# Optimization experiments

Hardware: AMD Instinct MI355X
Metric: run time of the kernel (lower is better)

## Reference

```python
import jax, jax.numpy as jnp
import numpy as np

N_NODES = 50000
N_EDGES = 600000
IN_DIM, HID, OUT_DIM = 128, 128, 64
LN_EPS = 1e-5


def setup_inputs() -> dict:
    key = jax.random.key(0)
    ks = jax.random.split(key, 10)
    def glorot(k, shape):
        lim = np.sqrt(6.0 / (shape[0] + shape[1]))
        return jax.random.uniform(k, shape, jnp.float32, -lim, lim)
    return {
        "x": jax.random.normal(ks[0], (N_NODES, IN_DIM), jnp.float32),
        "src": jax.random.randint(ks[1], (N_EDGES,), 0, N_NODES, jnp.int32),
        "dst": jax.random.randint(ks[2], (N_EDGES,), 0, N_NODES, jnp.int32),
        "W0": glorot(ks[3], (IN_DIM, HID)), "b0": jnp.zeros((HID,), jnp.float32),
        "W1": glorot(ks[4], (HID, HID)),    "b1": jnp.zeros((HID,), jnp.float32),
        "W2": glorot(ks[5], (HID, OUT_DIM)),"b2": jnp.zeros((OUT_DIM,), jnp.float32),
        "ln_scale": jnp.ones((HID,), jnp.float32),
        "ln_bias": jnp.zeros((HID,), jnp.float32),
    }


def _degree_norms(src, dst):
    ones = jnp.ones((src.shape[0],), jnp.float32)
    deg_out = jax.ops.segment_sum(ones, src, num_segments=N_NODES)
    deg_in = jax.ops.segment_sum(ones, dst, num_segments=N_NODES)
    # DGL clamps degree to min 1 for norm='both'
    out_norm = jnp.clip(deg_out, 1.0, None) ** -0.5
    in_norm = jnp.clip(deg_in, 1.0, None) ** -0.5
    return out_norm, in_norm


def _graph_conv(h, src, dst, out_norm, in_norm, W, b):
    # norm='both': scale src side, SpMM aggregate, scale dst side, then affine
    h = h * out_norm[:, None]
    h = h @ W  # apply weight first (mathematically identical, smaller messages when out<in)
    agg = jax.ops.segment_sum(h[src], dst, num_segments=N_NODES)  # [N, D]
    return agg * in_norm[:, None] + b


def _layernorm(h, scale, bias):
    mu = jnp.mean(h, axis=-1, keepdims=True)
    var = jnp.var(h, axis=-1, keepdims=True)
    return (h - mu) * jax.lax.rsqrt(var + LN_EPS) * scale + bias


def reference(x, src, dst, W0, b0, W1, b1, W2, b2, ln_scale, ln_bias):
    out_norm, in_norm = _degree_norms(src, dst)
    # dropout is identity in eval mode
    h = jax.nn.relu(_graph_conv(x, src, dst, out_norm, in_norm, W0, b0))
    h = _layernorm(h, ln_scale, ln_bias)
    h = jax.nn.relu(_graph_conv(h, src, dst, out_norm, in_norm, W1, b1))
    h = _layernorm(h, ln_scale, ln_bias)
    # last layer: encoding=True -> keep activation; no norm after last layer
    h = jax.nn.relu(_graph_conv(h, src, dst, out_norm, in_norm, W2, b2))
    return h
```

## Files before the change

kernel.cpp:

```cpp
#include <hip/hip_runtime.h>
#include <hip/hip_fp16.h>

#define NN 50000
#define NE 600000
#define LN_EPS 1e-5f
#define SCAN_B 49
#define RANGES 8
#define RSZ 6250
#define CHUNKS 30
#define CSZ 20000
#define HB (CHUNKS * RANGES)
#define GB ((NN + 63) / 64)

typedef __attribute__((ext_vector_type(8))) _Float16 half8;
typedef __attribute__((ext_vector_type(4))) float floatx4;

__device__ __align__(16) __half g_h0[NN * 128];
__device__ __align__(16) __half g_h1[NN * 128];
__device__ float g_out_norm[NN];
__device__ float g_in_norm[NN];
__device__ int g_rowptr[NN + 1];
__device__ int g_esrc[NE];
__device__ int g_blocksum[SCAN_B];
__device__ int g_perm[NN];
__device__ int g_dhist[SCAN_B * 256];
__device__ int g_pout[CHUNKS * NN];
__device__ int g_pin[CHUNKS * NN];
__device__ int g_base[CHUNKS * NN];
__device__ unsigned g_bar_count = 0;
__device__ unsigned g_bar_gen = 0;

__device__ __forceinline__ __half* hbuf(int i) { return i ? g_h1 : g_h0; }

__device__ __forceinline__ void gridbar(unsigned* expected) {
    __syncthreads();
    if (threadIdx.x == 0) {
        __threadfence();
        unsigned prev = __hip_atomic_fetch_add(&g_bar_count, 1u, __ATOMIC_ACQ_REL,
                                               __HIP_MEMORY_SCOPE_AGENT);
        if (prev == gridDim.x - 1) {
            __hip_atomic_store(&g_bar_count, 0u, __ATOMIC_RELAXED, __HIP_MEMORY_SCOPE_AGENT);
            __hip_atomic_fetch_add(&g_bar_gen, 1u, __ATOMIC_RELEASE, __HIP_MEMORY_SCOPE_AGENT);
        } else {
            while (__hip_atomic_load(&g_bar_gen, __ATOMIC_ACQUIRE, __HIP_MEMORY_SCOPE_AGENT) ==
                   *expected)
                __builtin_amdgcn_s_sleep(8);
        }
        __threadfence();
    }
    __syncthreads();
    (*expected)++;
}

__global__ __launch_bounds__(256) void k1_kernel(const int* __restrict__ src,
                                                 const int* __restrict__ dst,
                                                 const float* __restrict__ x,
                                                 const float* __restrict__ W0) {
    __shared__ __align__(16) int s_buf[2 * RSZ];
    const int tid = threadIdx.x;
    if (blockIdx.x < HB) {
        int* h_out = s_buf;
        int* h_in = s_buf + RSZ;
        int c = blockIdx.x / RANGES, r = blockIdx.x % RANGES;
        int lo = r * RSZ;
        for (int i = tid; i < RSZ; i += 256) { h_out[i] = 0; h_in[i] = 0; }
        __syncthreads();
        const int4* s4 = (const int4*)(src + c * CSZ);
        const int4* d4 = (const int4*)(dst + c * CSZ);
        for (int i = tid; i < CSZ / 4; i += 256) {
            int4 s = s4[i], d = d4[i];
            int v;
            v = s.x - lo; if ((unsigned)v < RSZ) atomicAdd(&h_out[v], 1);
            v = s.y - lo; if ((unsigned)v < RSZ) atomicAdd(&h_out[v], 1);
            v = s.z - lo; if ((unsigned)v < RSZ) atomicAdd(&h_out[v], 1);
            v = s.w - lo; if ((unsigned)v < RSZ) atomicAdd(&h_out[v], 1);
            v = d.x - lo; if ((unsigned)v < RSZ) atomicAdd(&h_in[v], 1);
            v = d.y - lo; if ((unsigned)v < RSZ) atomicAdd(&h_in[v], 1);
            v = d.z - lo; if ((unsigned)v < RSZ) atomicAdd(&h_in[v], 1);
            v = d.w - lo; if ((unsigned)v < RSZ) atomicAdd(&h_in[v], 1);
        }
        __syncthreads();
        for (int i = tid; i < RSZ; i += 256) {
            g_pout[c * NN + lo + i] = h_out[i];
            g_pin[c * NN + lo + i]  = h_in[i];
        }
    } else {
        _Float16* Wl = (_Float16*)s_buf;
        for (int e = tid; e < 128 * 128; e += 256) {
            int k = e >> 7, n = e & 127;
            Wl[(((k >> 3) * 128 + n) << 3) + (k & 7)] = (_Float16)W0[e];
        }
        __syncthreads();
        const int gb = blockIdx.x - HB;
        const int wv = tid >> 6, lane = tid & 63;
        const int quad = lane >> 4, mrow = lane & 15;
        const int rowbase = gb * 64 + wv * 16;
        const int arow0 = rowbase + mrow;
        const int arow = (arow0 < NN) ? arow0 : (NN - 1);
        floatx4 acc[8] = {};
#pragma unroll
        for (int kk = 0; kk < 4; ++kk) {
            const int k0 = kk * 32 + quad * 8;
            const float4* ap = (const float4*)(x + (size_t)arow * 128 + k0);
            float4 f0 = ap[0], f1 = ap[1];
            half8 afrag;
            afrag[0] = (_Float16)f0.x; afrag[1] = (_Float16)f0.y;
            afrag[2] = (_Float16)f0.z; afrag[3] = (_Float16)f0.w;
            afrag[4] = (_Float16)f1.x; afrag[5] = (_Float16)f1.y;
            afrag[6] = (_Float16)f1.z; afrag[7] = (_Float16)f1.w;
#pragma unroll
            for (int nt = 0; nt < 8; ++nt) {
                half8 bfrag = *(const half8*)&Wl[(((kk * 4 + quad) * 128 + nt * 16 + mrow) << 3)];
                acc[nt] = __builtin_amdgcn_mfma_f32_16x16x32_f16(afrag, bfrag, acc[nt], 0, 0, 0);
            }
        }
        __half* C = hbuf(0);
#pragma unroll
        for (int r = 0; r < 4; ++r) {
            int crow = rowbase + quad * 4 + r;
            if (crow < NN) {
#pragma unroll
                for (int nt = 0; nt < 8; ++nt)
                    C[(size_t)crow * 128 + nt * 16 + mrow] = __float2half_rn(acc[nt][r]);
            }
        }
    }
}

__global__ __launch_bounds__(1024) void mid_kernel() {
    __shared__ int wsum[16], woff[16];
    __shared__ int bscan[64];
    __shared__ int hist[256];
    __shared__ int cursor[256];
    __shared__ int cwsum[4], cwoff[4];
    unsigned expected = __hip_atomic_load(&g_bar_gen, __ATOMIC_RELAXED, __HIP_MEMORY_SCOPE_AGENT);
    const int b = blockIdx.x, t = threadIdx.x;
    const int lane = t & 63, wv = t >> 6;
    const int n = b * 1024 + t;
    if (t < 256) hist[t] = 0;
    int si = 0;
    if (n < NN) {
        int so = 0;
#pragma unroll
        for (int c = 0; c < CHUNKS; ++c) { so += g_pout[c * NN + n]; si += g_pin[c * NN + n]; }
        g_out_norm[n] = rsqrtf((float)max(so, 1));
        g_in_norm[n]  = rsqrtf((float)max(si, 1));
    }
    __syncthreads();
    int bin = min(si, 255);
    if (n < NN) atomicAdd(&hist[bin], 1);
    int inc = si;
#pragma unroll
    for (int off = 1; off < 64; off <<= 1) {
        int p = __shfl_up(inc, off, 64);
        if (lane >= off) inc += p;
    }
    if (lane == 63) wsum[wv] = inc;
    __syncthreads();
    if (t < 256) g_dhist[b * 256 + t] = hist[t];
    if (t < 16) {
        int x = wsum[t], y = x;
#pragma unroll
        for (int off = 1; off < 16; off <<= 1) {
            int p = __shfl_up(y, off, 16);
            if (t >= off) y += p;
        }
        woff[t] = y - x;
        if (t == 15) g_blocksum[b] = y;
    }
    gridbar(&expected);
    if (t < 64) {
        int own = (t < SCAN_B) ? g_blocksum[t] : 0;
        int v = own;
#pragma unroll
        for (int off = 1; off < 64; off <<= 1) {
            int p = __shfl_up(v, off, 64);
            if (t >= off) v += p;
        }
        bscan[t] = v - own;
        if (b == 0 && t == SCAN_B - 1) g_rowptr[NN] = v;
    }
    __syncthreads();
    int excl = (inc - si) + woff[wv] + bscan[b];
    if (n < NN) {
        g_rowptr[n] = excl;
        int run = excl;
#pragma unroll
        for (int c = 0; c < CHUNKS; ++c) {
            g_base[c * NN + n] = run;
            run += g_pin[c * NN + n];
        }
    }
    int cur = 0, tot = 0;
    if (t < 256) {
        for (int b2 = 0; b2 < SCAN_B; ++b2) {
            int h = g_dhist[b2 * 256 + t];
            cur += (b2 < b) ? h : 0;
            tot += h;
        }
    }
    int cinc = tot;
#pragma unroll
    for (int off = 1; off < 64; off <<= 1) {
        int p = __shfl_up(cinc, off, 64);
        if (lane >= off) cinc += p;
    }
    if (t < 256 && lane == 63) cwsum[wv] = cinc;
    __syncthreads();
    if (t < 4) {
        int x = cwsum[t], y = x;
#pragma unroll
        for (int off = 1; off < 4; off <<= 1) {
            int p = __shfl_up(y, off, 4);
            if (t >= off) y += p;
        }
        cwoff[t] = y - x;
    }
    __syncthreads();
    if (t < 256) cursor[t] = (cinc - tot) + cwoff[wv] + cur;
    __syncthreads();
    if (n < NN) {
        int pos = atomicAdd(&cursor[bin], 1);
        g_perm[pos] = n;
    }
}

__global__ __launch_bounds__(256) void place_lds_kernel(const int* __restrict__ src,
                                                        const int* __restrict__ dst) {
    __shared__ int cur[RSZ];
    int c = blockIdx.x / RANGES, r = blockIdx.x % RANGES;
    int lo = r * RSZ;
    for (int i = threadIdx.x; i < RSZ; i += 256) cur[i] = g_base[c * NN + lo + i];
    __syncthreads();
    const int4* s4 = (const int4*)(src + c * CSZ);
    const int4* d4 = (const int4*)(dst + c * CSZ);
    for (int i = threadIdx.x; i < CSZ / 4; i += 256) {
        int4 s = s4[i], d = d4[i];
        int v, p;
        v = d.x - lo; if ((unsigned)v < RSZ) { p = atomicAdd(&cur[v], 1); g_esrc[p] = s.x; }
        v = d.y - lo; if ((unsigned)v < RSZ) { p = atomicAdd(&cur[v], 1); g_esrc[p] = s.y; }
        v = d.z - lo; if ((unsigned)v < RSZ) { p = atomicAdd(&cur[v], 1); g_esrc[p] = s.z; }
        v = d.w - lo; if ((unsigned)v < RSZ) { p = atomicAdd(&cur[v], 1); g_esrc[p] = s.w; }
    }
}

template <int N>
__global__ __launch_bounds__(256) void gemm_mfma(int a_ib, int c_ib,
                                                 const float* __restrict__ Wg, int M) {
    constexpr int NT = N / 16;
    constexpr int LOGN = (N == 128) ? 7 : 6;
    __shared__ _Float16 Wl[128 * N];

    const int tid = threadIdx.x;
    for (int e = tid; e < 128 * N; e += 256) {
        int k = e >> LOGN, n = e & (N - 1);
        Wl[(((k >> 3) * N + n) << 3) + (k & 7)] = (_Float16)Wg[e];
    }
    __syncthreads();

    const int wv = tid >> 6, lane = tid & 63;
    const int quad = lane >> 4, mrow = lane & 15;
    const int rowbase = blockIdx.x * 64 + wv * 16;
    const int arow0 = rowbase + mrow;
    const int arow = (arow0 < M) ? arow0 : (M - 1);

    floatx4 acc[NT] = {};
    const __half* Ah = hbuf(a_ib);

#pragma unroll
    for (int kk = 0; kk < 4; ++kk) {
        const int k0 = kk * 32 + quad * 8;
        half8 afrag = *(const half8*)(Ah + (size_t)arow * 128 + k0);
#pragma unroll
        for (int nt = 0; nt < NT; ++nt) {
            half8 bfrag = *(const half8*)&Wl[(((kk * 4 + quad) * N + nt * 16 + mrow) << 3)];
            acc[nt] = __builtin_amdgcn_mfma_f32_16x16x32_f16(afrag, bfrag, acc[nt], 0, 0, 0);
        }
    }

    __half* C = hbuf(c_ib);
#pragma unroll
    for (int r = 0; r < 4; ++r) {
        int crow = rowbase + quad * 4 + r;
        if (crow < M) {
            float s = g_out_norm[crow];
#pragma unroll
            for (int nt = 0; nt < NT; ++nt) {
                float v = acc[nt][r] * s;
                C[(size_t)crow * N + nt * 16 + mrow] = __float2half_rn(v);
            }
        }
    }
}

__device__ __forceinline__ void acc_row(uint4 u, float wt,
                                        float& a0, float& a1, float& a2, float& a3,
                                        float& a4, float& a5, float& a6, float& a7) {
    float2 f0 = __half22float2(*(const __half2*)&u.x);
    float2 f1 = __half22float2(*(const __half2*)&u.y);
    float2 f2 = __half22float2(*(const __half2*)&u.z);
    float2 f3 = __half22float2(*(const __half2*)&u.w);
    a0 = fmaf(wt, f0.x, a0); a1 = fmaf(wt, f0.y, a1);
    a2 = fmaf(wt, f1.x, a2); a3 = fmaf(wt, f1.y, a3);
    a4 = fmaf(wt, f2.x, a4); a5 = fmaf(wt, f2.y, a5);
    a6 = fmaf(wt, f3.x, a6); a7 = fmaf(wt, f3.y, a7);
}

template <bool SC>
__global__ __launch_bounds__(256) void gather_ln_kernel(int s_ib, int d_ib,
                                                        const float* __restrict__ b,
                                                        const float* __restrict__ ln_s,
                                                        const float* __restrict__ ln_b) {
    int wave = threadIdx.x >> 6;
    int lane = threadIdx.x & 63;
    int sub = lane >> 4, sl = lane & 15;
    int idx = blockIdx.x * 16 + wave * 4 + sub;
    int node = g_perm[idx];
    const uint4* Hu = (const uint4*)hbuf(s_ib);
    int beg = g_rowptr[node], end = g_rowptr[node + 1];
    float a0 = 0.f, a1 = 0.f, a2 = 0.f, a3 = 0.f, a4 = 0.f, a5 = 0.f, a6 = 0.f, a7 = 0.f;
    int j = beg;
    for (; j + 7 < end; j += 8) {
        int ss[8]; uint4 uu[8]; float ww[8];
#pragma unroll
        for (int q = 0; q < 8; ++q) ss[q] = g_esrc[j + q];
#pragma unroll
        for (int q = 0; q < 8; ++q) uu[q] = Hu[ss[q] * 16 + sl];
#pragma unroll
        for (int q = 0; q < 8; ++q) ww[q] = SC ? g_out_norm[ss[q]] : 1.0f;
#pragma unroll
        for (int q = 0; q < 8; ++q) acc_row(uu[q], ww[q], a0, a1, a2, a3, a4, a5, a6, a7);
    }
    for (; j + 3 < end; j += 4) {
        int ss[4]; uint4 uu[4]; float ww[4];
#pragma unroll
        for (int q = 0; q < 4; ++q) ss[q] = g_esrc[j + q];
#pragma unroll
        for (int q = 0; q < 4; ++q) uu[q] = Hu[ss[q] * 16 + sl];
#pragma unroll
        for (int q = 0; q < 4; ++q) ww[q] = SC ? g_out_norm[ss[q]] : 1.0f;
#pragma unroll
        for (int q = 0; q < 4; ++q) acc_row(uu[q], ww[q], a0, a1, a2, a3, a4, a5, a6, a7);
    }
    for (; j < end; ++j) {
        int s0 = g_esrc[j];
        float w0 = SC ? g_out_norm[s0] : 1.0f;
        acc_row(Hu[s0 * 16 + sl], w0, a0, a1, a2, a3, a4, a5, a6, a7);
    }
    float nrm = g_in_norm[node];
    float4 bA = ((const float4*)b)[sl * 2], bB = ((const float4*)b)[sl * 2 + 1];
    float v0 = fmaxf(a0 * nrm + bA.x, 0.f), v1 = fmaxf(a1 * nrm + bA.y, 0.f);
    float v2 = fmaxf(a2 * nrm + bA.z, 0.f), v3 = fmaxf(a3 * nrm + bA.w, 0.f);
    float v4 = fmaxf(a4 * nrm + bB.x, 0.f), v5 = fmaxf(a5 * nrm + bB.y, 0.f);
    float v6 = fmaxf(a6 * nrm + bB.z, 0.f), v7 = fmaxf(a7 * nrm + bB.w, 0.f);
    float s = ((v0 + v1) + (v2 + v3)) + ((v4 + v5) + (v6 + v7));
    float sq = ((v0 * v0 + v1 * v1) + (v2 * v2 + v3 * v3)) +
               ((v4 * v4 + v5 * v5) + (v6 * v6 + v7 * v7));
#pragma unroll
    for (int off = 8; off > 0; off >>= 1) {
        s  += __shfl_xor(s, off, 64);
        sq += __shfl_xor(sq, off, 64);
    }
    float mean = s * (1.f / 128.f);
    float var = sq * (1.f / 128.f) - mean * mean;
    float inv = rsqrtf(var + LN_EPS);
    float4 lsA = ((const float4*)ln_s)[sl * 2], lsB = ((const float4*)ln_s)[sl * 2 + 1];
    float4 lbA = ((const float4*)ln_b)[sl * 2], lbB = ((const float4*)ln_b)[sl * 2 + 1];
    __half2 h0 = __floats2half2_rn((v0 - mean) * inv * lsA.x + lbA.x, (v1 - mean) * inv * lsA.y + lbA.y);
    __half2 h1 = __floats2half2_rn((v2 - mean) * inv * lsA.z + lbA.z, (v3 - mean) * inv * lsA.w + lbA.w);
    __half2 h2 = __floats2half2_rn((v4 - mean) * inv * lsB.x + lbB.x, (v5 - mean) * inv * lsB.y + lbB.y);
    __half2 h3 = __floats2half2_rn((v6 - mean) * inv * lsB.z + lbB.z, (v7 - mean) * inv * lsB.w + lbB.w);
    uint4 o = make_uint4(*(const unsigned int*)&h0, *(const unsigned int*)&h1,
                         *(const unsigned int*)&h2, *(const unsigned int*)&h3);
    ((uint4*)hbuf(d_ib))[node * 16 + sl] = o;
}

__global__ __launch_bounds__(256) void GCN_63831803953156_kernel(int s_ib,
                                                                 const float* __restrict__ b2,
                                                                 float* __restrict__ out) {
    int wave = threadIdx.x >> 6;
    int lane = threadIdx.x & 63;
    int sub = lane >> 3, sl = lane & 7;
    int idx = blockIdx.x * 32 + wave * 8 + sub;
    if (idx >= NN) return;
    int node = g_perm[idx];
    const uint4* Hu = (const uint4*)hbuf(s_ib);
    int beg = g_rowptr[node], end = g_rowptr[node + 1];
    float a0 = 0.f, a1 = 0.f, a2 = 0.f, a3 = 0.f, a4 = 0.f, a5 = 0.f, a6 = 0.f, a7 = 0.f;
    int j = beg;
    for (; j + 7 < end; j += 8) {
        int ss[8]; uint4 uu[8];
#pragma unroll
        for (int q = 0; q < 8; ++q) ss[q] = g_esrc[j + q];
#pragma unroll
        for (int q = 0; q < 8; ++q) uu[q] = Hu[ss[q] * 8 + sl];
#pragma unroll
        for (int q = 0; q < 8; ++q) acc_row(uu[q], 1.0f, a0, a1, a2, a3, a4, a5, a6, a7);
    }
    for (; j + 3 < end; j += 4) {
        int ss[4]; uint4 uu[4];
#pragma unroll
        for (int q = 0; q < 4; ++q) ss[q] = g_esrc[j + q];
#pragma unroll
        for (int q = 0; q < 4; ++q) uu[q] = Hu[ss[q] * 8 + sl];
#pragma unroll
        for (int q = 0; q < 4; ++q) acc_row(uu[q], 1.0f, a0, a1, a2, a3, a4, a5, a6, a7);
    }
    for (; j < end; ++j)
        acc_row(Hu[g_esrc[j] * 8 + sl], 1.0f, a0, a1, a2, a3, a4, a5, a6, a7);
    float nrm = g_in_norm[node];
    float4 bA = ((const float4*)b2)[sl * 2], bB = ((const float4*)b2)[sl * 2 + 1];
    float4 oA, oB;
    oA.x = fmaxf(a0 * nrm + bA.x, 0.f); oA.y = fmaxf(a1 * nrm + bA.y, 0.f);
    oA.z = fmaxf(a2 * nrm + bA.z, 0.f); oA.w = fmaxf(a3 * nrm + bA.w, 0.f);
    oB.x = fmaxf(a4 * nrm + bB.x, 0.f); oB.y = fmaxf(a5 * nrm + bB.y, 0.f);
    oB.z = fmaxf(a6 * nrm + bB.z, 0.f); oB.w = fmaxf(a7 * nrm + bB.w, 0.f);
    ((float4*)out)[node * 16 + sl * 2] = oA;
    ((float4*)out)[node * 16 + sl * 2 + 1] = oB;
}

extern "C" void kernel_launch(void* const* d_in, const int* in_sizes, int n_in,
                              void* d_out, int out_size, void* d_ws, size_t ws_size,
                              hipStream_t stream) {
    const float* x   = (const float*)d_in[0];
    const int* src   = (const int*)d_in[1];
    const int* dst   = (const int*)d_in[2];
    const float* W0  = (const float*)d_in[3];
    const float* b0  = (const float*)d_in[4];
    const float* W1  = (const float*)d_in[5];
    const float* b1  = (const float*)d_in[6];
    const float* W2  = (const float*)d_in[7];
    const float* b2  = (const float*)d_in[8];
    const float* ln_s = (const float*)d_in[9];
    const float* ln_b = (const float*)d_in[10];
    (void)d_ws; (void)ws_size; (void)in_sizes; (void)n_in; (void)out_size;

    k1_kernel<<<HB + GB, 256, 0, stream>>>(src, dst, x, W0);
    mid_kernel<<<SCAN_B, 1024, 0, stream>>>();
    place_lds_kernel<<<HB, 256, 0, stream>>>(src, dst);

    gather_ln_kernel<true><<<NN / 16, 256, 0, stream>>>(0, 1, b0, ln_s, ln_b);

    gemm_mfma<128><<<GB, 256, 0, stream>>>(1, 0, W1, NN);
    gather_ln_kernel<false><<<NN / 16, 256, 0, stream>>>(0, 1, b1, ln_s, ln_b);

    gemm_mfma<64><<<GB, 256, 0, stream>>>(1, 0, W2, NN);
    GCN_63831803953156_kernel<<<(NN + 31) / 32, 256, 0, stream>>>(0, b2, (float*)d_out);
}
```

Baseline: 231.0 us.

## Split first-layer GEMM tiles between histogram and edge-placement kernels

The first GEMM (x @ W0) was computed entirely alongside the degree-histogram blocks in the first kernel. Now only the first 390 row tiles run there, and the remaining tiles are appended as extra blocks to the edge-placement kernel (renamed k3), so the dense work fills idle CUs in both scatter-heavy phases. The GEMM tile body is factored into a shared device function. The k3 LDS buffer grows to 32 KB to hold the W0 copy, which may cut occupancy for the placement blocks.

```diff
diff --git a/kernel.cpp b/kernel.cpp
--- a/kernel.cpp
+++ b/kernel.cpp
@@ -11,6 +11,7 @@
 #define CSZ 20000
 #define HB (CHUNKS * RANGES)
 #define GB ((NN + 63) / 64)
+#define G1 390
 
 typedef __attribute__((ext_vector_type(8))) _Float16 half8;
 typedef __attribute__((ext_vector_type(4))) float floatx4;
@@ -50,6 +51,48 @@
     }
     __syncthreads();
     (*expected)++;
+}
+
+__device__ __forceinline__ void gemm0_tile(_Float16* Wl, const float* __restrict__ x,
+                                           const float* __restrict__ W0, int tile) {
+    const int tid = threadIdx.x;
+    for (int e = tid; e < 128 * 128; e += 256) {
+        int k = e >> 7, n = e & 127;
+        Wl[(((k >> 3) * 128 + n) << 3) + (k & 7)] = (_Float16)W0[e];
+    }
+    __syncthreads();
+    const int wv = tid >> 6, lane = tid & 63;
+    const int quad = lane >> 4, mrow = lane & 15;
+    const int rowbase = tile * 64 + wv * 16;
+    const int arow0 = rowbase + mrow;
+    const int arow = (arow0 < NN) ? arow0 : (NN - 1);
+    floatx4 acc[8] = {};
+#pragma unroll
+    for (int kk = 0; kk < 4; ++kk) {
+        const int k0 = kk * 32 + quad * 8;
+        const float4* ap = (const float4*)(x + (size_t)arow * 128 + k0);
+        float4 f0 = ap[0], f1 = ap[1];
+        half8 afrag;
+        afrag[0] = (_Float16)f0.x; afrag[1] = (_Float16)f0.y;
+        afrag[2] = (_Float16)f0.z; afrag[3] = (_Float16)f0.w;
+        afrag[4] = (_Float16)f1.x; afrag[5] = (_Float16)f1.y;
+        afrag[6] = (_Float16)f1.z; afrag[7] = (_Float16)f1.w;
+#pragma unroll
+        for (int nt = 0; nt < 8; ++nt) {
+            half8 bfrag = *(const half8*)&Wl[(((kk * 4 + quad) * 128 + nt * 16 + mrow) << 3)];
+            acc[nt] = __builtin_amdgcn_mfma_f32_16x16x32_f16(afrag, bfrag, acc[nt], 0, 0, 0);
+        }
+    }
+    __half* C = hbuf(0);
+#pragma unroll
+    for (int r = 0; r < 4; ++r) {
+        int crow = rowbase + quad * 4 + r;
+        if (crow < NN) {
+#pragma unroll
+            for (int nt = 0; nt < 8; ++nt)
+                C[(size_t)crow * 128 + nt * 16 + mrow] = __float2half_rn(acc[nt][r]);
+        }
+    }
 }
 
 __global__ __launch_bounds__(256) void k1_kernel(const int* __restrict__ src,
@@ -85,45 +128,7 @@
             g_pin[c * NN + lo + i]  = h_in[i];
         }
     } else {
-        _Float16* Wl = (_Float16*)s_buf;
-        for (int e = tid; e < 128 * 128; e += 256) {
-            int k = e >> 7, n = e & 127;
-            Wl[(((k >> 3) * 128 + n) << 3) + (k & 7)] = (_Float16)W0[e];
-        }
-        __syncthreads();
-        const int gb = blockIdx.x - HB;
-        const int wv = tid >> 6, lane = tid & 63;
-        const int quad = lane >> 4, mrow = lane & 15;
-        const int rowbase = gb * 64 + wv * 16;
-        const int arow0 = rowbase + mrow;
-        const int arow = (arow0 < NN) ? arow0 : (NN - 1);
-        floatx4 acc[8] = {};
-#pragma unroll
-        for (int kk = 0; kk < 4; ++kk) {
-            const int k0 = kk * 32 + quad * 8;
-            const float4* ap = (const float4*)(x + (size_t)arow * 128 + k0);
-            float4 f0 = ap[0], f1 = ap[1];
-            half8 afrag;
-            afrag[0] = (_Float16)f0.x; afrag[1] = (_Float16)f0.y;
-            afrag[2] = (_Float16)f0.z; afrag[3] = (_Float16)f0.w;
-            afrag[4] = (_Float16)f1.x; afrag[5] = (_Float16)f1.y;
-            afrag[6] = (_Float16)f1.z; afrag[7] = (_Float16)f1.w;
-#pragma unroll
-            for (int nt = 0; nt < 8; ++nt) {
-                half8 bfrag = *(const half8*)&Wl[(((kk * 4 + quad) * 128 + nt * 16 + mrow) << 3)];
-                acc[nt] = __builtin_amdgcn_mfma_f32_16x16x32_f16(afrag, bfrag, acc[nt], 0, 0, 0);
-            }
-        }
-        __half* C = hbuf(0);
-#pragma unroll
-        for (int r = 0; r < 4; ++r) {
-            int crow = rowbase + quad * 4 + r;
-            if (crow < NN) {
-#pragma unroll
-                for (int nt = 0; nt < 8; ++nt)
-                    C[(size_t)crow * 128 + nt * 16 + mrow] = __float2half_rn(acc[nt][r]);
-            }
-        }
+        gemm0_tile((_Float16*)s_buf, x, W0, blockIdx.x - HB);
     }
 }
 
@@ -225,22 +230,30 @@
     }
 }
 
-__global__ __launch_bounds__(256) void place_lds_kernel(const int* __restrict__ src,
-                                                        const int* __restrict__ dst) {
-    __shared__ int cur[RSZ];
-    int c = blockIdx.x / RANGES, r = blockIdx.x % RANGES;
-    int lo = r * RSZ;
-    for (int i = threadIdx.x; i < RSZ; i += 256) cur[i] = g_base[c * NN + lo + i];
-    __syncthreads();
-    const int4* s4 = (const int4*)(src + c * CSZ);
-    const int4* d4 = (const int4*)(dst + c * CSZ);
-    for (int i = threadIdx.x; i < CSZ / 4; i += 256) {
-        int4 s = s4[i], d = d4[i];
-        int v, p;
-        v = d.x - lo; if ((unsigned)v < RSZ) { p = atomicAdd(&cur[v], 1); g_esrc[p] = s.x; }
-        v = d.y - lo; if ((unsigned)v < RSZ) { p = atomicAdd(&cur[v], 1); g_esrc[p] = s.y; }
-        v = d.z - lo; if ((unsigned)v < RSZ) { p = atomicAdd(&cur[v], 1); g_esrc[p] = s.z; }
-        v = d.w - lo; if ((unsigned)v < RSZ) { p = atomicAdd(&cur[v], 1); g_esrc[p] = s.w; }
+__global__ __launch_bounds__(256) void k3_kernel(const int* __restrict__ src,
+                                                 const int* __restrict__ dst,
+                                                 const float* __restrict__ x,
+                                                 const float* __restrict__ W0) {
+    __shared__ __align__(16) int s_buf[8192];
+    const int tid = threadIdx.x;
+    if (blockIdx.x < HB) {
+        int* cur = s_buf;
+        int c = blockIdx.x / RANGES, r = blockIdx.x % RANGES;
+        int lo = r * RSZ;
+        for (int i = tid; i < RSZ; i += 256) cur[i] = g_base[c * NN + lo + i];
+        __syncthreads();
+        const int4* s4 = (const int4*)(src + c * CSZ);
+        const int4* d4 = (const int4*)(dst + c * CSZ);
+        for (int i = tid; i < CSZ / 4; i += 256) {
+            int4 s = s4[i], d = d4[i];
+            int v, p;
+            v = d.x - lo; if ((unsigned)v < RSZ) { p = atomicAdd(&cur[v], 1); g_esrc[p] = s.x; }
+            v = d.y - lo; if ((unsigned)v < RSZ) { p = atomicAdd(&cur[v], 1); g_esrc[p] = s.y; }
+            v = d.z - lo; if ((unsigned)v < RSZ) { p = atomicAdd(&cur[v], 1); g_esrc[p] = s.z; }
+            v = d.w - lo; if ((unsigned)v < RSZ) { p = atomicAdd(&cur[v], 1); g_esrc[p] = s.w; }
+        }
+    } else {
+        gemm0_tile((_Float16*)s_buf, x, W0, blockIdx.x - HB + G1);
     }
 }
 
@@ -435,9 +448,9 @@
     const float* ln_b = (const float*)d_in[10];
     (void)d_ws; (void)ws_size; (void)in_sizes; (void)n_in; (void)out_size;
 
-    k1_kernel<<<HB + GB, 256, 0, stream>>>(src, dst, x, W0);
+    k1_kernel<<<HB + G1, 256, 0, stream>>>(src, dst, x, W0);
     mid_kernel<<<SCAN_B, 1024, 0, stream>>>();
-    place_lds_kernel<<<HB, 256, 0, stream>>>(src, dst);
+    k3_kernel<<<HB + (GB - G1), 256, 0, stream>>>(src, dst, x, W0);
 
     gather_ln_kernel<true><<<NN / 16, 256, 0, stream>>>(0, 1, b0, ln_s, ln_b);
 
```

Measured after the change: 232.7 us. Within noise of the previous version (+0.7%).
